# Performance work log

Measured on AMD Instinct MI355X. Metric: run time of the kernel, lower is better.

## Reference

```python
import jax, jax.numpy as jnp
import numpy as np


def logdotexp(A, B):
    # Stable log-domain matmul: logsumexp_k(A[m,k] + B[k,n]) without the 3D broadcast.
    amax = jnp.max(A, axis=1, keepdims=True)   # [m,1]
    bmax = jnp.max(B, axis=0, keepdims=True)   # [1,n]
    return jnp.log(jnp.exp(A - amax) @ jnp.exp(B - bmax)) + amax + bmax


def setup_inputs() -> dict:
    key = jax.random.key(0)
    k1, k2, k3, k4 = jax.random.split(key, 4)
    C, S, N, T = 64, 256, 2000, 500
    return {
        "unnormalized_state_init": jax.random.normal(k1, (C, S), dtype=jnp.float32),
        "unnormalized_chain_weights": jax.random.normal(k2, (T, C), dtype=jnp.float32),
        "unnormalized_emission_matrix": jax.random.normal(k3, (S, N), dtype=jnp.float32),
        "unnormalized_transition_matrix": jax.random.normal(k4, (S, S), dtype=jnp.float32),
        "emissions_mask": jnp.ones((S, N), dtype=jnp.float32),
    }


def reference(unnormalized_state_init, unnormalized_chain_weights,
              unnormalized_emission_matrix, unnormalized_transition_matrix,
              emissions_mask):
    log_state_init = jax.nn.log_softmax(unnormalized_state_init, axis=1)        # [C,S]
    log_chain_weights = jax.nn.log_softmax(unnormalized_chain_weights, axis=1)  # [T,C]
    log_E_ = jax.nn.log_softmax(unnormalized_emission_matrix, axis=1) + jnp.log(emissions_mask)
    log_E = log_E_ - jax.scipy.special.logsumexp(log_E_, axis=1, keepdims=True)  # [S,N]
    log_Tm = jax.nn.log_softmax(unnormalized_transition_matrix, axis=1)          # [S,S]

    T = unnormalized_chain_weights.shape[0]
    C, S = log_state_init.shape
    N = log_E.shape[1]

    def step(h, _):
        h_next = logdotexp(h, log_Tm)  # [C,S]
        return h_next, h_next

    _, hs = jax.lax.scan(step, log_state_init, None, length=T - 1)  # [T-1,C,S]
    log_hidden = jnp.concatenate([log_state_init[None], hs], axis=0)  # [T,C,S]

    # Emission for all timesteps at once via one big stabilized matmul.
    log_obs_ = logdotexp(log_hidden.reshape(T * C, S), log_E).reshape(T, C, N)  # [T,C,N]
    log_obs = jax.scipy.special.logsumexp(log_obs_ + log_chain_weights[:, :, None], axis=1)  # [T,N]
    return log_obs, log_obs_, log_hidden
```

## Files before the change

kernel.cpp:

```cpp
#include <hip/hip_runtime.h>
#include <cstddef>

typedef unsigned short u16;
typedef float f32x4 __attribute__((ext_vector_type(4)));
typedef short bf16x8 __attribute__((ext_vector_type(8)));

#define SDIM 256
#define CDIM 64
#define NDIM 2000
#define TDIM 500

#define MAT  (SDIM*SDIM)
#define HMAT (CDIM*SDIM)

#define OFF_POW    0u
#define OFF_HEADS  (OFF_POW + MAT)
#define OFF_CW     (OFF_HEADS + HMAT)
#define OFF_EPROB  (OFF_CW + 32000u)
#define OFF_ET     (OFF_EPROB + 512000u)
#define OFF_PT     (OFF_ET + 262144u)
#define OFF_PPB    (OFF_PT + 819200u)
#define OFF_RPB    (OFF_PPB + 819200u)
#define OFF_RPT    (OFF_RPB + 131072u)
#define OFF_HDB    (OFF_RPT + 131072u)
#define OFF_HB     (OFF_HDB + 163840u)

#define U16OFF(X) ((unsigned)((X) * 2u))

#define OUT_OBSB  1000000u
#define OUT_HIDB  65000000u

#define TP 260

__device__ __forceinline__ float waveMax(float v) {
#pragma unroll
  for (int o = 32; o >= 1; o >>= 1) v = fmaxf(v, __shfl_xor(v, o));
  return v;
}
__device__ __forceinline__ float waveSum(float v) {
#pragma unroll
  for (int o = 32; o >= 1; o >>= 1) v += __shfl_xor(v, o);
  return v;
}
__device__ __forceinline__ u16 f2b(float f) {
  union { float f; unsigned u; } x; x.f = f;
  return (u16)((x.u + 0x7fffu + ((x.u >> 16) & 1u)) >> 16);
}
__device__ __forceinline__ float b2f(u16 b) {
  union { unsigned u; float f; } x; x.u = ((unsigned)b) << 16;
  return x.f;
}

__global__ __launch_bounds__(256) void prep_prob(
    const float* __restrict__ si, const float* __restrict__ cw,
    const float* __restrict__ em, const float* __restrict__ tm,
    const float* __restrict__ mask, float* __restrict__ ws) {
  int b = blockIdx.x;
  const float* src; const float* msk = nullptr; float* dst; int len;
  if (b < 64)       { src = si + b*SDIM;                 dst = ws + OFF_HEADS + b*SDIM; len = SDIM; }
  else if (b < 564) { int r = b - 64;  src = cw + r*64;  dst = ws + OFF_CW + r*64;      len = 64;   }
  else if (b < 820) { int r = b - 564; src = tm + (size_t)r*SDIM; dst = ws + OFF_POW + (size_t)r*SDIM; len = SDIM; }
  else              { int r = b - 820; src = em + (size_t)r*NDIM; dst = ws + OFF_EPROB + (size_t)r*NDIM; len = NDIM; msk = mask + (size_t)r*NDIM; }
  int tid = threadIdx.x;
  __shared__ float rA[4], rB[4];
  float m = -INFINITY;
  for (int i = tid; i < len; i += 256) {
    float v = src[i];
    if (msk) v += __logf(msk[i]);
    m = fmaxf(m, v);
  }
  m = waveMax(m);
  if ((tid & 63) == 0) rA[tid >> 6] = m;
  __syncthreads();
  m = fmaxf(fmaxf(rA[0], rA[1]), fmaxf(rA[2], rA[3]));
  float s = 0.f;
  for (int i = tid; i < len; i += 256) {
    float v = src[i];
    if (msk) v += __logf(msk[i]);
    s += __expf(v - m);
  }
  s = waveSum(s);
  if ((tid & 63) == 0) rB[tid >> 6] = s;
  __syncthreads();
  s = rB[0] + rB[1] + rB[2] + rB[3];
  float inv = 1.f / s;
  for (int i = tid; i < len; i += 256) {
    float v = src[i];
    if (msk) v += __logf(msk[i]);
    dst[i] = __expf(v - m) * inv;
  }
}

__device__ void trans_tile(const float* __restrict__ src, int ldn, int nReal,
                           u16* __restrict__ dst, int n0, int k0,
                           float (*tile)[65]) {
  int tid = threadIdx.x;
  {
    int kk = tid >> 2, p = tid & 3;
    const float* s = src + (size_t)(k0 + kk)*ldn + n0 + p*16;
#pragma unroll
    for (int i = 0; i < 16; ++i) {
      int n = n0 + p*16 + i;
      tile[p*16 + i][kk] = (n < nReal) ? s[i] : 0.f;
    }
  }
  __syncthreads();
  {
    int rr = tid >> 2, kq = (tid & 3) * 16;
    unsigned w[8];
#pragma unroll
    for (int i = 0; i < 8; ++i)
      w[i] = (unsigned)f2b(tile[rr][kq + 2*i]) | ((unsigned)f2b(tile[rr][kq + 2*i + 1]) << 16);
    uint4* d = (uint4*)(dst + (size_t)(n0 + rr)*256 + k0 + kq);
    d[0] = *(uint4*)&w[0];
    d[1] = *(uint4*)&w[4];
  }
}

__global__ __launch_bounds__(256) void prep2(float* __restrict__ ws) {
  __shared__ float tile[64][65];
  int b = blockIdx.x, tid = threadIdx.x;
  if (b < 128) {
    trans_tile(ws + OFF_EPROB, NDIM, NDIM, (u16*)ws + U16OFF(OFF_ET), (b >> 2)*64, (b & 3)*64, tile);
  } else if (b < 144) {
    int t = b - 128;
    trans_tile(ws + OFF_POW, SDIM, SDIM, (u16*)ws + U16OFF(OFF_PT), (t >> 2)*64, (t & 3)*64, tile);
  } else if (b < 152) {
    int t = b - 144;
    const float* s = ws + OFF_POW + t*8192;
    unsigned* d = (unsigned*)((u16*)ws + U16OFF(OFF_PPB)) + t*4096;
    for (int i = tid; i < 4096; i += 256) {
      float2 v = *(const float2*)(s + 2*i);
      d[i] = (unsigned)f2b(v.x) | ((unsigned)f2b(v.y) << 16);
    }
  } else {
    int t = b - 152;
    const float* s = ws + OFF_HEADS + t*8192;
    unsigned* d = (unsigned*)((u16*)ws + U16OFF(OFF_HDB)) + t*4096;
    for (int i = tid; i < 4096; i += 256) {
      float2 v = *(const float2*)(s + 2*i);
      d[i] = (unsigned)f2b(v.x) | ((unsigned)f2b(v.y) << 16);
    }
  }
}

__device__ __forceinline__ void stageAB(int tid, const u16* __restrict__ gA,
                                        const u16* __restrict__ gB, int kc,
                                        char* ldsA, char* ldsB) {
#pragma unroll
  for (int p = 0; p < 2; ++p) {
    int row = p*32 + (tid >> 3), slot = tid & 7;
    uint4 v = *(const uint4*)((const char*)gA + (size_t)row*512 + kc*128 + slot*16);
    *(uint4*)(ldsA + row*128 + ((slot*16) ^ ((row & 7) << 4))) = v;
  }
#pragma unroll
  for (int p = 0; p < 8; ++p) {
    int row = p*32 + (tid >> 3), slot = tid & 7;
    uint4 v = *(const uint4*)((const char*)gB + (size_t)row*512 + kc*128 + slot*16);
    *(uint4*)(ldsB + row*128 + ((slot*16) ^ ((row & 7) << 4))) = v;
  }
}

__device__ __forceinline__ void mfma_block(int g16, int c16, int wid,
                                           const char* ldsA, const char* ldsB,
                                           f32x4 (&acc)[4][4]) {
#pragma unroll
  for (int ks = 0; ks < 2; ++ks) {
    bf16x8 af[4], bfr[4];
    int kb = ks*64 + g16*16;
#pragma unroll
    for (int mf = 0; mf < 4; ++mf) {
      int row = mf*16 + c16;
      af[mf] = *(const bf16x8*)(ldsA + row*128 + (kb ^ ((row & 7) << 4)));
    }
#pragma unroll
    for (int nf = 0; nf < 4; ++nf) {
      int n = wid*64 + nf*16 + c16;
      bfr[nf] = *(const bf16x8*)(ldsB + n*128 + (kb ^ ((n & 7) << 4)));
    }
#pragma unroll
    for (int mf = 0; mf < 4; ++mf)
#pragma unroll
      for (int nf = 0; nf < 4; ++nf)
        acc[mf][nf] = __builtin_amdgcn_mfma_f32_16x16x32_bf16(af[mf], bfr[nf], acc[mf][nf], 0, 0, 0);
  }
}

struct CJobs {
  int n;
  unsigned a[12], b[12], cp[12], ct[12];
  unsigned short tiles[12];
};

__global__ __launch_bounds__(256) void chain_mfma(float* __restrict__ ws, CJobs jb) {
  int t = blockIdx.x, k = 0;
  while (t >= jb.tiles[k]) { t -= jb.tiles[k]; ++k; }
  int r0 = t * 64;
  u16* wsu = (u16*)ws;
  const u16* gA = wsu + jb.a[k] + (size_t)r0*256;
  const u16* gB = wsu + jb.b[k];
  u16* cp = wsu + jb.cp[k] + (size_t)r0*256;
  bool hasCT = (jb.ct[k] != 0xFFFFFFFFu);
  u16* ctB = wsu + (hasCT ? jb.ct[k] : 0u);
  int tid = threadIdx.x;
  __shared__ __align__(16) char smem[41600];
  char* ldsA = smem; char* ldsB = smem + 8192;
  int wid = tid >> 6, lane = tid & 63, g16 = lane >> 4, c16 = lane & 15;
  f32x4 acc[4][4];
#pragma unroll
  for (int mf = 0; mf < 4; ++mf)
#pragma unroll
    for (int nf = 0; nf < 4; ++nf) acc[mf][nf] = {0.f, 0.f, 0.f, 0.f};
  stageAB(tid, gA, gB, 0, ldsA, ldsB);
  __syncthreads();
  for (int kc = 0; kc < 4; ++kc) {
    mfma_block(g16, c16, wid, ldsA, ldsB, acc);
    __syncthreads();
    if (kc < 3) { stageAB(tid, gA, gB, kc + 1, ldsA, ldsB); __syncthreads(); }
  }
  float* tile = (float*)smem;
#pragma unroll
  for (int p = 0; p < 2; ++p) {
    if (p) __syncthreads();
#pragma unroll
    for (int mf = 2*p; mf < 2*p + 2; ++mf)
#pragma unroll
      for (int r = 0; r < 4; ++r) {
        int lrow = mf*16 + g16*4 + r - 32*p;
#pragma unroll
        for (int nf = 0; nf < 4; ++nf) {
          int n = wid*64 + nf*16 + c16;
          tile[lrow*TP + n] = acc[mf][nf][r];
        }
      }
    __syncthreads();
#pragma unroll
    for (int r8 = 0; r8 < 8; ++r8) {
      int row = wid*8 + r8;
      int m = 32*p + row;
      f32x4 v = *(const f32x4*)&tile[row*TP + lane*4];
      uint2 w;
      w.x = (unsigned)f2b(v[0]) | ((unsigned)f2b(v[1]) << 16);
      w.y = (unsigned)f2b(v[2]) | ((unsigned)f2b(v[3]) << 16);
      *(uint2*)(cp + (size_t)m*256 + lane*4) = w;
    }
    if (hasCT) {
#pragma unroll
      for (int it = 0; it < 4; ++it) {
        int n = it*64 + lane;
        unsigned w[16];
#pragma unroll
        for (int j = 0; j < 16; ++j)
          w[j] = (unsigned)f2b(tile[2*j*TP + n]) | ((unsigned)f2b(tile[(2*j+1)*TP + n]) << 16);
        uint4* d = (uint4*)(ctB + (size_t)n*256 + r0 + 32*p);
        d[0] = *(uint4*)&w[0];
        d[1] = *(uint4*)&w[4];
        d[2] = *(uint4*)&w[8];
        d[3] = *(uint4*)&w[12];
      }
    }
  }
}

__global__ __launch_bounds__(256) void fill_mfma(float* __restrict__ ws_f, float* __restrict__ out) {
  int tt = blockIdx.x;
  int b = tt / 25, j = tt % 25;
  int tid = threadIdx.x;
  float* hid = out + OUT_HIDB + (size_t)tt*HMAT;
  u16* hb = (u16*)ws_f + U16OFF(OFF_HB) + (size_t)tt*HMAT;
  const u16* gA = (u16*)ws_f + U16OFF(OFF_HDB) + (size_t)b*HMAT;
  if (j == 0) {
    for (int i = tid; i < HMAT; i += 256) {
      u16 hv = gA[i];
      hid[i] = __logf(b2f(hv));
      hb[i] = hv;
    }
    return;
  }
  const u16* gB = (u16*)ws_f + U16OFF(OFF_PT) + (size_t)(j - 1)*MAT;
  __shared__ __align__(16) char smem[41600];
  char* ldsA = smem; char* ldsB = smem + 8192;
  int wid = tid >> 6, lane = tid & 63, g16 = lane >> 4, c16 = lane & 15;
  f32x4 acc[4][4];
#pragma unroll
  for (int mf = 0; mf < 4; ++mf)
#pragma unroll
    for (int nf = 0; nf < 4; ++nf) acc[mf][nf] = {0.f, 0.f, 0.f, 0.f};
  stageAB(tid, gA, gB, 0, ldsA, ldsB);
  __syncthreads();
  for (int kc = 0; kc < 4; ++kc) {
    mfma_block(g16, c16, wid, ldsA, ldsB, acc);
    __syncthreads();
    if (kc < 3) { stageAB(tid, gA, gB, kc + 1, ldsA, ldsB); __syncthreads(); }
  }
  float* tile = (float*)smem;
#pragma unroll
  for (int p = 0; p < 2; ++p) {
    if (p) __syncthreads();
#pragma unroll
    for (int mf = 2*p; mf < 2*p + 2; ++mf)
#pragma unroll
      for (int r = 0; r < 4; ++r) {
        int lrow = mf*16 + g16*4 + r - 32*p;
#pragma unroll
        for (int nf = 0; nf < 4; ++nf) {
          int n = wid*64 + nf*16 + c16;
          tile[lrow*TP + n] = acc[mf][nf][r];
        }
      }
    __syncthreads();
#pragma unroll
    for (int r8 = 0; r8 < 8; ++r8) {
      int row = wid*8 + r8;
      int c = 32*p + row;
      f32x4 v = *(const f32x4*)&tile[row*TP + lane*4];
      f32x4 lg = {__logf(v[0]), __logf(v[1]), __logf(v[2]), __logf(v[3])};
      __builtin_nontemporal_store(lg, (f32x4*)(hid + (size_t)c*256 + lane*4));
      uint2 w;
      w.x = (unsigned)f2b(v[0]) | ((unsigned)f2b(v[1]) << 16);
      w.y = (unsigned)f2b(v[2]) | ((unsigned)f2b(v[3]) << 16);
      *(uint2*)(hb + (size_t)c*256 + lane*4) = w;
    }
  }
}

__global__ __launch_bounds__(256) void emission_mfma(const float* __restrict__ ws_f, float* __restrict__ out) {
  int tt = blockIdx.y, n0 = blockIdx.x * 256;
  int tid = threadIdx.x;
  const u16* gA = (const u16*)ws_f + U16OFF(OFF_HB) + (size_t)tt*HMAT;
  const u16* gB = (const u16*)ws_f + U16OFF(OFF_ET) + (size_t)n0*256;
  __shared__ __align__(16) char smem[41600];
  __shared__ float sCw[64];
  char* ldsA = smem; char* ldsB = smem + 8192;
  if (tid < 64) sCw[tid] = ws_f[OFF_CW + tt*64 + tid];
  int wid = tid >> 6, lane = tid & 63, g16 = lane >> 4, c16 = lane & 15;
  f32x4 acc[4][4];
#pragma unroll
  for (int mf = 0; mf < 4; ++mf)
#pragma unroll
    for (int nf = 0; nf < 4; ++nf) acc[mf][nf] = {0.f, 0.f, 0.f, 0.f};
  stageAB(tid, gA, gB, 0, ldsA, ldsB);
  __syncthreads();
  for (int kc = 0; kc < 4; ++kc) {
    mfma_block(g16, c16, wid, ldsA, ldsB, acc);
    __syncthreads();
    if (kc < 3) { stageAB(tid, gA, gB, kc + 1, ldsA, ldsB); __syncthreads(); }
  }
  float s[4] = {0.f, 0.f, 0.f, 0.f};
  int nn[4];
#pragma unroll
  for (int nf = 0; nf < 4; ++nf) nn[nf] = n0 + wid*64 + nf*16 + c16;
#pragma unroll
  for (int mf = 0; mf < 4; ++mf)
#pragma unroll
    for (int r = 0; r < 4; ++r) {
      float wc = sCw[mf*16 + g16*4 + r];
#pragma unroll
      for (int nf = 0; nf < 4; ++nf) s[nf] += acc[mf][nf][r] * wc;
    }
#pragma unroll
  for (int nf = 0; nf < 4; ++nf) {
    s[nf] += __shfl_xor(s[nf], 16);
    s[nf] += __shfl_xor(s[nf], 32);
  }
  if (g16 == 0) {
#pragma unroll
    for (int nf = 0; nf < 4; ++nf)
      if (nn[nf] < NDIM) out[(size_t)tt*NDIM + nn[nf]] = __logf(s[nf]);
  }
  float* obsb = out + OUT_OBSB + (size_t)tt*CDIM*NDIM;
  float* tile = (float*)smem;
  bool okc = (n0 + (lane + 1)*4 <= NDIM);
#pragma unroll
  for (int p = 0; p < 2; ++p) {
    __syncthreads();
#pragma unroll
    for (int mf = 2*p; mf < 2*p + 2; ++mf)
#pragma unroll
      for (int r = 0; r < 4; ++r) {
        int lrow = mf*16 + g16*4 + r - 32*p;
#pragma unroll
        for (int nf = 0; nf < 4; ++nf) {
          int n = wid*64 + nf*16 + c16;
          tile[lrow*TP + n] = acc[mf][nf][r];
        }
      }
    __syncthreads();
#pragma unroll
    for (int r8 = 0; r8 < 8; ++r8) {
      int row = wid*8 + r8;
      int c = 32*p + row;
      if (okc) {
        f32x4 v = *(const f32x4*)&tile[row*TP + lane*4];
        f32x4 lg = {__logf(v[0]), __logf(v[1]), __logf(v[2]), __logf(v[3])};
        __builtin_nontemporal_store(lg, (f32x4*)(obsb + (size_t)c*NDIM + n0 + lane*4));
      }
    }
  }
}

extern "C" void kernel_launch(void* const* d_in, const int* in_sizes, int n_in,
                              void* d_out, int out_size, void* d_ws, size_t ws_size,
                              hipStream_t stream) {
  const float* si   = (const float*)d_in[0];
  const float* cw   = (const float*)d_in[1];
  const float* em   = (const float*)d_in[2];
  const float* tm   = (const float*)d_in[3];
  const float* mask = (const float*)d_in[4];
  float* out = (float*)d_out;
  float* ws  = (float*)d_ws;
  dim3 blk(256);

  prep_prob<<<dim3(1076), blk, 0, stream>>>(si, cw, em, tm, mask, ws);
  prep2<<<dim3(154), blk, 0, stream>>>(ws);

  auto ppb = [](int i){ return U16OFF(OFF_PPB) + (unsigned)i*MAT; };
  auto pt  = [](int i){ return U16OFF(OFF_PT)  + (unsigned)i*MAT; };
  auto rpb = [](int i){ return U16OFF(OFF_RPB) + (unsigned)i*MAT; };
  auto rpt = [](int i){ return U16OFF(OFF_RPT) + (unsigned)i*MAT; };
  auto hdb = [](int b){ return U16OFF(OFF_HDB) + (unsigned)b*HMAT; };

  CJobs jb;
  int ji = 0, total = 0;
  auto add = [&](unsigned a, unsigned b, unsigned cp, unsigned ct, int M) {
    jb.a[ji] = a; jb.b[ji] = b; jb.cp[ji] = cp; jb.ct[ji] = ct;
    jb.tiles[ji] = (M == 256) ? 4 : 1; total += jb.tiles[ji]; ++ji;
  };
  auto launch = [&]() {
    jb.n = ji;
    chain_mfma<<<dim3(total), blk, 0, stream>>>(ws, jb);
    ji = 0; total = 0;
  };
  const unsigned NOCT = 0xFFFFFFFFu;

  add(ppb(0), pt(0), ppb(1), pt(1), 256); launch();
  add(ppb(1), pt(0), ppb(2), pt(2), 256);
  add(ppb(1), pt(1), ppb(3), pt(3), 256); launch();
  for (int i = 0; i < 4; ++i) add(ppb(3), pt(i), ppb(4+i), pt(4+i), 256); launch();
  for (int i = 0; i < 8; ++i) add(ppb(7), pt(i), ppb(8+i), pt(8+i), 256); launch();
  for (int i = 0; i < 9; ++i) add(ppb(15), pt(i), ppb(16+i), pt(16+i), 256); launch();

  add(hdb(0), pt(24), hdb(1), NOCT, 64);
  add(ppb(24), pt(24), rpb(0), rpt(0), 256); launch();
  add(hdb(0), rpt(0), hdb(2), NOCT, 64);
  add(hdb(1), rpt(0), hdb(3), NOCT, 64);
  add(rpb(0), rpt(0), rpb(1), rpt(1), 256); launch();
  for (int i = 0; i < 4; ++i) add(hdb(i), rpt(1), hdb(4+i), NOCT, 64);
  add(rpb(1), rpt(1), rpb(2), rpt(2), 256); launch();
  for (int i = 0; i < 8; ++i) add(hdb(i), rpt(2), hdb(8+i), NOCT, 64);
  add(rpb(2), rpt(2), rpb(3), rpt(3), 256); launch();
  for (int i = 0; i < 4; ++i) add(hdb(i), rpt(3), hdb(16+i), NOCT, 64); launch();

  fill_mfma<<<dim3(500), blk, 0, stream>>>(ws, out);

  emission_mfma<<<dim3(8, 500), blk, 0, stream>>>(ws, out);
}
```

Baseline: 478.5 us.

## Stage GEMM tiles with direct global-to-LDS loads and remap block ordering

```diff
diff --git a/kernel.cpp b/kernel.cpp
--- a/kernel.cpp
+++ b/kernel.cpp
@@ -49,6 +49,12 @@
 __device__ __forceinline__ float b2f(u16 b) {
   union { unsigned u; float f; } x; x.u = ((unsigned)b) << 16;
   return x.f;
+}
+
+__device__ __forceinline__ void gload16(const void* g, void* l) {
+  __builtin_amdgcn_global_load_lds(
+      (const __attribute__((address_space(1))) void*)g,
+      (__attribute__((address_space(3))) void*)l, 16, 0, 0);
 }
 
 __global__ __launch_bounds__(256) void prep_prob(
@@ -147,17 +153,20 @@
 __device__ __forceinline__ void stageAB(int tid, const u16* __restrict__ gA,
                                         const u16* __restrict__ gB, int kc,
                                         char* ldsA, char* ldsB) {
+  int w = tid >> 6, lane = tid & 63;
+  int srow = lane >> 3;
+  int sslot = (lane & 7) ^ srow;
 #pragma unroll
   for (int p = 0; p < 2; ++p) {
-    int row = p*32 + (tid >> 3), slot = tid & 7;
-    uint4 v = *(const uint4*)((const char*)gA + (size_t)row*512 + kc*128 + slot*16);
-    *(uint4*)(ldsA + row*128 + ((slot*16) ^ ((row & 7) << 4))) = v;
+    int rbase = p*32 + w*8;
+    gload16((const char*)gA + (size_t)(rbase + srow)*512 + kc*128 + sslot*16,
+            ldsA + rbase*128);
   }
 #pragma unroll
   for (int p = 0; p < 8; ++p) {
-    int row = p*32 + (tid >> 3), slot = tid & 7;
-    uint4 v = *(const uint4*)((const char*)gB + (size_t)row*512 + kc*128 + slot*16);
-    *(uint4*)(ldsB + row*128 + ((slot*16) ^ ((row & 7) << 4))) = v;
+    int rbase = p*32 + w*8;
+    gload16((const char*)gB + (size_t)(rbase + srow)*512 + kc*128 + sslot*16,
+            ldsB + rbase*128);
   }
 }
 
@@ -263,8 +272,10 @@
 }
 
 __global__ __launch_bounds__(256) void fill_mfma(float* __restrict__ ws_f, float* __restrict__ out) {
-  int tt = blockIdx.x;
-  int b = tt / 25, j = tt % 25;
+  int bid = blockIdx.x;
+  int j = bid & 31, b = bid >> 5;
+  if (j >= 25) return;
+  int tt = b*25 + j;
   int tid = threadIdx.x;
   float* hid = out + OUT_HIDB + (size_t)tt*HMAT;
   u16* hb = (u16*)ws_f + U16OFF(OFF_HB) + (size_t)tt*HMAT;
@@ -325,7 +336,10 @@
 }
 
 __global__ __launch_bounds__(256) void emission_mfma(const float* __restrict__ ws_f, float* __restrict__ out) {
-  int tt = blockIdx.y, n0 = blockIdx.x * 256;
+  int bid = blockIdx.x;
+  int tt = bid & 511, n0i = bid >> 9;
+  if (tt >= TDIM) return;
+  int n0 = n0i * 256;
   int tid = threadIdx.x;
   const u16* gA = (const u16*)ws_f + U16OFF(OFF_HB) + (size_t)tt*HMAT;
   const u16* gB = (const u16*)ws_f + U16OFF(OFF_ET) + (size_t)n0*256;
@@ -451,7 +465,7 @@
   add(rpb(2), rpt(2), rpb(3), rpt(3), 256); launch();
   for (int i = 0; i < 4; ++i) add(hdb(i), rpt(3), hdb(16+i), NOCT, 64); launch();
 
-  fill_mfma<<<dim3(500), blk, 0, stream>>>(ws, out);
-
-  emission_mfma<<<dim3(8, 500), blk, 0, stream>>>(ws, out);
-}
+  fill_mfma<<<dim3(640), blk, 0, stream>>>(ws, out);
+
+  emission_mfma<<<dim3(4096), blk, 0, stream>>>(ws, out);
+}
```

New measurement: 481.7 us. About the same (+0.7%).
